# Optimization experiments

Measured on AMD Instinct MI355X. Metric: run time of the kernel, lower is better.

Reference implementation:

```python
import jax, jax.numpy as jnp
import numpy as np

B = 8
SHAPE = (4, 16, 16)   # latent video shape; S = prod = 1024
S = 1024
AE = 64               # ae_embed_dim
D = 768               # embed_dim
F = 3072              # mlp_dim
H = 12                # num_heads (heads are re-merged before the score matmul!)
L = 12                # num_layers
C = 17                # n_classes
OUT = 1024            # out_dim
EPS = 1e-6
HD = D // H


def setup_inputs() -> dict:
    key = jax.random.key(0)
    ks = iter(jax.random.split(key, 64))

    def p(shape, s=0.02):
        return jax.random.normal(next(ks), shape, jnp.float32) * s

    inp = {
        'x': jax.random.normal(next(ks), (B, *SHAPE, AE), jnp.float32),
        'mask': jnp.tril(jnp.ones((S, S), bool)),  # causal
        'label': jax.nn.one_hot(jax.random.randint(next(ks), (B,), 0, C), C, dtype=jnp.float32),
        'dense_in_w': p((D, AE)), 'dense_in_b': jnp.zeros((D,), jnp.float32),
        'sos': p((D,)),
        # BroadcastPositionBiases: embed_dim=768 split into 3 chunks of 256
        'pos0': p((SHAPE[0], D // 3)), 'pos1': p((SHAPE[1], D // 3)), 'pos2': p((SHAPE[2], D // 3)),
        'ln1_sw': p((L, D, C)), 'ln1_bw': p((L, D, C)),
        'qkv_w': p((L, 3 * D, D)), 'qkv_b': jnp.zeros((L, 3 * D), jnp.float32),
        'ao1_w': p((L, D, D)), 'ao1_b': jnp.zeros((L, D), jnp.float32),  # DotProductAttention.out_proj
        'ao2_w': p((L, D, D)), 'ao2_b': jnp.zeros((L, D), jnp.float32),  # MultiHeadAttention.out_proj
        'ln2_sw': p((L, D, C)), 'ln2_bw': p((L, D, C)),
        'mlp_w1': p((L, F, D)), 'mlp_b1': jnp.zeros((L, F), jnp.float32),
        'mlp_w2': p((L, D, F)), 'mlp_b2': jnp.zeros((L, D), jnp.float32),
        'lnf_sw': p((D, C)), 'lnf_bw': p((D, C)),
        'out_w': p((OUT, D)), 'out_b': jnp.zeros((OUT,), jnp.float32),
    }
    return inp


def cond_ln(x, cond, sw, bw):
    # conditional LayerNorm: mul = rsqrt(var+eps)*(1+Linear(cond)), bias = Linear(cond)
    mean = jnp.mean(x, axis=-1, keepdims=True)
    var = jnp.mean((x - mean) ** 2, axis=-1, keepdims=True)
    scale = cond @ sw.T   # [B, D]
    bias = cond @ bw.T    # [B, D]
    mul = jax.lax.rsqrt(var + EPS) * (1.0 + scale[:, None, :])
    return (x - mean) * mul + bias[:, None, :]


def pos_bias(embs, shape):
    n = len(shape)
    outs = []
    for i, e in enumerate(embs):
        sh = [1] * n + [e.shape[-1]]
        sh[i] = shape[i]
        outs.append(jnp.broadcast_to(e.reshape(sh), tuple(shape) + (e.shape[-1],)))
    return jnp.concatenate(outs, axis=-1).reshape(-1, sum(e.shape[-1] for e in embs))  # [S, D]


def attn_block(h, mask, qkv_w, qkv_b, o1_w, o1_b, o2_w, o2_b):
    Bn, Sn, Dn = h.shape
    qkv = h @ qkv_w.T + qkv_b                       # [B, S, 3D]
    qkv = qkv.reshape(Bn, Sn, H, 3 * HD)            # per-head [q|k|v] layout
    q = qkv[..., :HD].reshape(Bn, Sn, Dn)           # heads re-merged BEFORE scores
    k = qkv[..., HD:2 * HD].reshape(Bn, Sn, Dn)
    v = qkv[..., 2 * HD:].reshape(Bn, Sn, Dn)
    # NOTE: scaling uses full embed_dim (module quirk), not head_dim
    scores = jnp.einsum('bqd,bkd->bqk', q * (float(Dn) ** -0.5), k)
    scores = jnp.where(mask[None, :, :], scores, -jnp.inf)
    w = jax.nn.softmax(scores, axis=-1)
    out = jnp.einsum('bqk,bkd->bqd', w, v)
    out = out @ o1_w.T + o1_b                        # DotProductAttention.out_proj
    out = out @ o2_w.T + o2_b                        # MultiHeadAttention.out_proj (applied twice)
    return out


def _forward(x, mask, label, dense_in_w, dense_in_b, sos, pos0, pos1, pos2,
             ln1_sw, ln1_bw, qkv_w, qkv_b, ao1_w, ao1_b, ao2_w, ao2_b,
             ln2_sw, ln2_bw, mlp_w1, mlp_b1, mlp_w2, mlp_b2,
             lnf_sw, lnf_bw, out_w, out_b):
    Bn = x.shape[0]
    old_shape = x.shape[1:-1]
    h = x.reshape(Bn, -1, x.shape[-1]) @ dense_in_w.T + dense_in_b   # [B, S, D]
    # right shift with learned SOS token
    h = jnp.concatenate([jnp.broadcast_to(sos, (Bn, 1, D)), h[:, :-1]], axis=1)
    pb = pos_bias([pos0, pos1, pos2], old_shape)                     # [S, D]
    h = h + pb[None, :h.shape[1]]
    for l in range(L):
        hn = cond_ln(h, label, ln1_sw[l], ln1_bw[l])
        h = h + attn_block(hn, mask, qkv_w[l], qkv_b[l], ao1_w[l], ao1_b[l], ao2_w[l], ao2_b[l])
        hn = cond_ln(h, label, ln2_sw[l], ln2_bw[l])
        m = hn @ mlp_w1[l].T + mlp_b1[l]
        m = jax.nn.sigmoid(1.702 * m) * m           # GELU2
        m = m @ mlp_w2[l].T + mlp_b2[l]
        h = h + m
    h = cond_ln(h, label, lnf_sw, lnf_bw)
    out = h @ out_w.T + out_b                        # [B, S, OUT]
    return out.reshape(Bn, *old_shape, out.shape[-1])


def reference(x, mask, label, dense_in_w, dense_in_b, sos, pos0, pos1, pos2,
              ln1_sw, ln1_bw, qkv_w, qkv_b, ao1_w, ao1_b, ao2_w, ao2_b,
              ln2_sw, ln2_bw, mlp_w1, mlp_b1, mlp_w2, mlp_b2,
              lnf_sw, lnf_bw, out_w, out_b):
    return _forward(x, mask, label, dense_in_w, dense_in_b, sos, pos0, pos1, pos2,
                    ln1_sw, ln1_bw, qkv_w, qkv_b, ao1_w, ao1_b, ao2_w, ao2_b,
                    ln2_sw, ln2_bw, mlp_w1, mlp_b1, mlp_w2, mlp_b2,
                    lnf_sw, lnf_bw, out_w, out_b)
```

## Files before the change

### kernel.cpp

```cpp
#include <hip/hip_runtime.h>

typedef __bf16 bf16;
typedef __bf16 bf16x8 __attribute__((ext_vector_type(8)));
typedef __bf16 bf16x4 __attribute__((ext_vector_type(4)));
typedef float  f32x4  __attribute__((ext_vector_type(4)));

#define DEV __device__ __forceinline__

DEV void gload_lds16(const bf16* g, bf16* l) {
    __builtin_amdgcn_global_load_lds(
        (__attribute__((address_space(1))) void*)g,
        (__attribute__((address_space(3))) void*)l, 16, 0, 0);
}

enum { M_QKV, M_SCORES, M_PV, M_RESID, M_GELU, M_OUT, M_WM };

template<int MODE>
__global__ __launch_bounds__(256)
void gemm_k(const bf16* __restrict__ A, const bf16* __restrict__ B,
            int M, int N, int K,
            long long batchA, long long batchB, long long batchC,
            const float* __restrict__ bias,
            bf16* __restrict__ Cb, float* __restrict__ Cf,
            bf16* __restrict__ qp, bf16* __restrict__ kp, bf16* __restrict__ vp)
{
    const int bm = blockIdx.x, bn = blockIdx.y, bz = blockIdx.z;
    int kTiles = K >> 5;

    const int tid = threadIdx.x, wid = tid >> 6, lane = tid & 63;
    const bf16* Ab = A + (long long)bz * batchA + (long long)bm * 128 * K;
    const bf16* Bb = B + (long long)bz * batchB + (long long)bn * 128 * K;

    __shared__ __align__(16) bf16 sA[2][4096];
    __shared__ __align__(16) bf16 sB[2][4096];

    const int srow = wid * 16 + (lane >> 2);
    const int scol = (lane & 3) * 8;
    const long long aoff = (long long)srow * K + scol;

    auto stage = [&](int buf, int kt) {
        const bf16* ga = Ab + (long long)kt * 32;
        const bf16* gb = Bb + (long long)kt * 32;
        gload_lds16(ga + aoff,            &sA[buf][(wid * 16) * 32]);
        gload_lds16(ga + aoff + 64LL * K, &sA[buf][(64 + wid * 16) * 32]);
        gload_lds16(gb + aoff,            &sB[buf][(wid * 16) * 32]);
        gload_lds16(gb + aoff + 64LL * K, &sB[buf][(64 + wid * 16) * 32]);
    };

    f32x4 acc[4][4];
#pragma unroll
    for (int m = 0; m < 4; ++m)
#pragma unroll
        for (int n = 0; n < 4; ++n) acc[m][n] = (f32x4){0.f, 0.f, 0.f, 0.f};

    stage(0, 0);
    __syncthreads();

    const int wr = wid >> 1, wc = wid & 1;
    const int arow = wr * 64 + (lane & 15);
    const int brow = wc * 64 + (lane & 15);
    const int koff = (lane >> 4) * 8;

    for (int kt = 0; kt < kTiles; ++kt) {
        const int cur = kt & 1;
        if (kt + 1 < kTiles) stage(cur ^ 1, kt + 1);
        bf16x8 af[4], bfr[4];
#pragma unroll
        for (int m = 0; m < 4; ++m)
            af[m] = *(const bf16x8*)&sA[cur][(arow + m * 16) * 32 + koff];
#pragma unroll
        for (int n = 0; n < 4; ++n)
            bfr[n] = *(const bf16x8*)&sB[cur][(brow + n * 16) * 32 + koff];
#pragma unroll
        for (int m = 0; m < 4; ++m)
#pragma unroll
            for (int n = 0; n < 4; ++n)
                acc[m][n] = __builtin_amdgcn_mfma_f32_16x16x32_bf16(af[m], bfr[n], acc[m][n], 0, 0, 0);
        __syncthreads();
    }

    const int cr0 = bm * 128 + wr * 64 + (lane >> 4) * 4;
    const int cc0 = bn * 128 + wc * 64 + (lane & 15);
#pragma unroll
    for (int m = 0; m < 4; ++m) {
#pragma unroll
        for (int n = 0; n < 4; ++n) {
            const int col = cc0 + n * 16;
#pragma unroll
            for (int r = 0; r < 4; ++r) {
                const int row = cr0 + m * 16 + r;
                float v = acc[m][n][r];
                if (MODE == M_QKV) {
                    v += bias[col];
                    int hd = col / 192, rr = col % 192;
                    int b = row >> 10, s = row & 1023;
                    if (rr < 64)
                        qp[(long long)row * 768 + hd * 64 + rr] = (bf16)(v * 0.03608439182435161f);
                    else if (rr < 128)
                        kp[(long long)row * 768 + hd * 64 + (rr - 64)] = (bf16)v;
                    else
                        vp[((long long)b * 768 + hd * 64 + (rr - 128)) * 1024 + s] = (bf16)v;
                } else if (MODE == M_GELU) {
                    float xg = v + bias[col];
                    Cb[(long long)row * N + col] = (bf16)(xg / (1.f + __expf(-1.702f * xg)));
                } else if (MODE == M_RESID) {
                    long long idx = (long long)row * N + col;
                    Cf[idx] += v + bias[col];
                } else if (MODE == M_WM) {
                    Cb[(long long)bz * batchC + (long long)row * N + col] = (bf16)v;
                } else {
                    Cf[(long long)row * N + col] = v + bias[col];
                }
            }
        }
    }
}

template<int MODE>
__global__ __launch_bounds__(256)
void gemm64_k(const bf16* __restrict__ A, const bf16* __restrict__ B,
              int M, int N, int K,
              long long batchA, long long batchB, long long batchC,
              const float* __restrict__ bias,
              bf16* __restrict__ Cb, float* __restrict__ Cf)
{
    const int bm = blockIdx.x, bn = blockIdx.y, bz = blockIdx.z;
    if (MODE == M_SCORES && 2 * bn > bm) return;
    int kTiles = K >> 5;
    if (MODE == M_PV) {
        int lim = 2 * bm + 2;
        if (lim < kTiles) kTiles = lim;
    }

    const int tid = threadIdx.x, wid = tid >> 6, lane = tid & 63;
    const bf16* Ab = A + (long long)bz * batchA + (long long)bm * 64 * K;
    const bf16* Bb = B + (long long)bz * batchB + (long long)bn * 128 * K;

    __shared__ __align__(16) bf16 sA[2][2048];
    __shared__ __align__(16) bf16 sB[2][4096];

    const int srow = wid * 16 + (lane >> 2);
    const int scol = (lane & 3) * 8;
    const long long aoff = (long long)srow * K + scol;

    auto stage = [&](int buf, int kt) {
        const bf16* ga = Ab + (long long)kt * 32;
        const bf16* gb = Bb + (long long)kt * 32;
        gload_lds16(ga + aoff,            &sA[buf][(wid * 16) * 32]);
        gload_lds16(gb + aoff,            &sB[buf][(wid * 16) * 32]);
        gload_lds16(gb + aoff + 64LL * K, &sB[buf][(64 + wid * 16) * 32]);
    };

    f32x4 acc[2][4];
#pragma unroll
    for (int m = 0; m < 2; ++m)
#pragma unroll
        for (int n = 0; n < 4; ++n) acc[m][n] = (f32x4){0.f, 0.f, 0.f, 0.f};

    stage(0, 0);
    __syncthreads();

    const int wr = wid >> 1, wc = wid & 1;
    const int arow = wr * 32 + (lane & 15);
    const int brow = wc * 64 + (lane & 15);
    const int koff = (lane >> 4) * 8;

    for (int kt = 0; kt < kTiles; ++kt) {
        const int cur = kt & 1;
        if (kt + 1 < kTiles) stage(cur ^ 1, kt + 1);
        bf16x8 af[2], bfr[4];
#pragma unroll
        for (int m = 0; m < 2; ++m)
            af[m] = *(const bf16x8*)&sA[cur][(arow + m * 16) * 32 + koff];
#pragma unroll
        for (int n = 0; n < 4; ++n)
            bfr[n] = *(const bf16x8*)&sB[cur][(brow + n * 16) * 32 + koff];
#pragma unroll
        for (int m = 0; m < 2; ++m)
#pragma unroll
            for (int n = 0; n < 4; ++n)
                acc[m][n] = __builtin_amdgcn_mfma_f32_16x16x32_bf16(af[m], bfr[n], acc[m][n], 0, 0, 0);
        __syncthreads();
    }

    const int cr0 = bm * 64 + wr * 32 + (lane >> 4) * 4;
    const int cc0 = bn * 128 + wc * 64 + (lane & 15);
#pragma unroll
    for (int m = 0; m < 2; ++m) {
#pragma unroll
        for (int n = 0; n < 4; ++n) {
            const int col = cc0 + n * 16;
#pragma unroll
            for (int r = 0; r < 4; ++r) {
                const int row = cr0 + m * 16 + r;
                float v = acc[m][n][r];
                if (MODE == M_SCORES || MODE == M_PV) {
                    Cb[(long long)bz * batchC + (long long)row * N + col] = (bf16)v;
                } else {
                    Cf[(long long)row * N + col] = v + bias[col];
                }
            }
        }
    }
}

__global__ __launch_bounds__(256)
void cvt_bf16_k(const float* __restrict__ in, bf16* __restrict__ out, int n4)
{
    int i = blockIdx.x * 256 + threadIdx.x;
    if (i >= n4) return;
    float4 f = ((const float4*)in)[i];
    bf16x4 o = { (bf16)f.x, (bf16)f.y, (bf16)f.z, (bf16)f.w };
    ((bf16x4*)out)[i] = o;
}

__global__ __launch_bounds__(256)
void transpose_cvt_k(const float* __restrict__ in, bf16* __restrict__ out, int n)
{
    __shared__ float t[32][33];
    const int l = blockIdx.z;
    const int r0 = blockIdx.y * 32, c0 = blockIdx.x * 32;
    const float* src = in + (long long)l * n * n;
    bf16* dst = out + (long long)l * n * n;
    const int tx = threadIdx.x & 31, ty = threadIdx.x >> 5;
#pragma unroll
    for (int i = 0; i < 32; i += 8)
        t[ty + i][tx] = src[(long long)(r0 + ty + i) * n + c0 + tx];
    __syncthreads();
#pragma unroll
    for (int i = 0; i < 32; i += 8)
        dst[(long long)(c0 + ty + i) * n + r0 + tx] = (bf16)t[tx][ty + i];
}

__global__ __launch_bounds__(256)
void bias_merge_k(const float* __restrict__ o2w, const float* __restrict__ o1b,
                  const float* __restrict__ o2b, float* __restrict__ bm, int total)
{
    const int wid = threadIdx.x >> 6, lane = threadIdx.x & 63;
    const int idx = blockIdx.x * 4 + wid;
    if (idx >= total) return;
    const int l = idx / 768, a = idx - l * 768;
    const float* wrow = o2w + ((long long)l * 768 + a) * 768;
    const float* brow = o1b + (long long)l * 768;
    float s = 0.f;
#pragma unroll
    for (int j = 0; j < 12; ++j) {
        int c = j * 64 + lane;
        s += wrow[c] * brow[c];
    }
#pragma unroll
    for (int o = 32; o; o >>= 1) s += __shfl_down(s, o);
    if (lane == 0) bm[idx] = s + o2b[(long long)l * 768 + a];
}

__global__ __launch_bounds__(256)
void cond_proj_k(const float* __restrict__ label, const float* __restrict__ sw,
                 const float* __restrict__ bw, float* __restrict__ scale,
                 float* __restrict__ bias, int total)
{
    int idx = blockIdx.x * 256 + threadIdx.x;
    if (idx >= total) return;
    int l = idx / 6144;
    int rem = idx - l * 6144;
    int b = rem / 768, d = rem - (rem / 768) * 768;
    const float* lab = label + b * 17;
    const float* swp = sw + ((long long)l * 768 + d) * 17;
    const float* bwp = bw + ((long long)l * 768 + d) * 17;
    float s = 0.f, bb = 0.f;
#pragma unroll
    for (int c = 0; c < 17; ++c) { float lv = lab[c]; s += lv * swp[c]; bb += lv * bwp[c]; }
    scale[idx] = s;
    bias[idx]  = bb;
}

__global__ __launch_bounds__(256)
void shift_pos_k(const float* __restrict__ xe, const float* __restrict__ sos,
                 const float* __restrict__ p0, const float* __restrict__ p1,
                 const float* __restrict__ p2, float* __restrict__ h)
{
    const int s = blockIdx.x, b = blockIdx.y;
    const int i0 = s >> 8, i1 = (s >> 4) & 15, i2 = s & 15;
    const float* xr = xe + ((long long)b * 1024 + (s - 1)) * 768;
#pragma unroll
    for (int j = 0; j < 3; ++j) {
        const int d = j * 256 + threadIdx.x;
        float v = (s == 0) ? sos[d] : xr[d];
        float pbv = (d < 256) ? p0[i0 * 256 + d]
                  : (d < 512) ? p1[i1 * 256 + (d - 256)]
                              : p2[i2 * 256 + (d - 512)];
        h[((long long)b * 1024 + s) * 768 + d] = v + pbv;
    }
}

__global__ __launch_bounds__(256)
void cond_ln_k(const float* __restrict__ h, const float* __restrict__ scale,
               const float* __restrict__ bias, bf16* __restrict__ out)
{
    const long long row = (long long)blockIdx.y * 1024 + blockIdx.x;
    const int b = blockIdx.y;
    const float* hr = h + row * 768;
    float v[3], sum = 0.f, sq = 0.f;
#pragma unroll
    for (int j = 0; j < 3; ++j) {
        v[j] = hr[j * 256 + threadIdx.x];
        sum += v[j]; sq += v[j] * v[j];
    }
    __shared__ float sm[8];
#pragma unroll
    for (int o = 32; o; o >>= 1) { sum += __shfl_down(sum, o); sq += __shfl_down(sq, o); }
    const int wid = threadIdx.x >> 6;
    if ((threadIdx.x & 63) == 0) { sm[wid] = sum; sm[4 + wid] = sq; }
    __syncthreads();
    sum = sm[0] + sm[1] + sm[2] + sm[3];
    sq  = sm[4] + sm[5] + sm[6] + sm[7];
    const float mean = sum * (1.f / 768.f);
    const float var  = sq * (1.f / 768.f) - mean * mean;
    const float rs   = rsqrtf(var + 1e-6f);
    const float* sc = scale + (long long)b * 768;
    const float* bi = bias  + (long long)b * 768;
    bf16* orow = out + row * 768;
#pragma unroll
    for (int j = 0; j < 3; ++j) {
        const int d = j * 256 + threadIdx.x;
        orow[d] = (bf16)((v[j] - mean) * rs * (1.f + sc[d]) + bi[d]);
    }
}

__global__ __launch_bounds__(256)
void softmax_k(bf16* __restrict__ P)
{
    const int i = blockIdx.x, b = blockIdx.y;
    bf16* row = P + ((long long)b * 1024 + i) * 1024;
    const int len = i + 1;
    const int lim = (i | 63) + 1;
    float v[4], mx = -1e30f;
#pragma unroll
    for (int j = 0; j < 4; ++j) {
        int c = j * 256 + threadIdx.x;
        v[j] = (c < len) ? (float)row[c] : -1e30f;
        mx = fmaxf(mx, v[j]);
    }
    __shared__ float sm[8];
#pragma unroll
    for (int o = 32; o; o >>= 1) mx = fmaxf(mx, __shfl_down(mx, o));
    const int wid = threadIdx.x >> 6;
    if ((threadIdx.x & 63) == 0) sm[wid] = mx;
    __syncthreads();
    mx = fmaxf(fmaxf(sm[0], sm[1]), fmaxf(sm[2], sm[3]));
    float s = 0.f;
#pragma unroll
    for (int j = 0; j < 4; ++j) {
        v[j] = __expf(v[j] - mx);
        s += ((j * 256 + threadIdx.x) < len) ? v[j] : 0.f;
    }
#pragma unroll
    for (int o = 32; o; o >>= 1) s += __shfl_down(s, o);
    if ((threadIdx.x & 63) == 0) sm[4 + wid] = s;
    __syncthreads();
    s = sm[4] + sm[5] + sm[6] + sm[7];
    const float inv = 1.f / s;
#pragma unroll
    for (int j = 0; j < 4; ++j) {
        int c = j * 256 + threadIdx.x;
        if (c < lim) row[c] = (c < len) ? (bf16)(v[j] * inv) : (bf16)0.f;
    }
}

__global__ __launch_bounds__(256)
void fill_k(float* o, int n, float v)
{
    int i = blockIdx.x * 256 + threadIdx.x;
    if (i < n) o[i] = v;
}

extern "C" void kernel_launch(void* const* d_in, const int* in_sizes, int n_in,
                              void* d_out, int out_size, void* d_ws, size_t ws_size,
                              hipStream_t stream)
{
    (void)in_sizes; (void)n_in;
    const float* x     = (const float*)d_in[0];
    const float* label = (const float*)d_in[2];
    const float* dw    = (const float*)d_in[3];
    const float* db    = (const float*)d_in[4];
    const float* sos   = (const float*)d_in[5];
    const float* p0    = (const float*)d_in[6];
    const float* p1    = (const float*)d_in[7];
    const float* p2    = (const float*)d_in[8];
    const float* ln1sw = (const float*)d_in[9];
    const float* ln1bw = (const float*)d_in[10];
    const float* qkvw  = (const float*)d_in[11];
    const float* qkvb  = (const float*)d_in[12];
    const float* ao1w  = (const float*)d_in[13];
    const float* ao1b  = (const float*)d_in[14];
    const float* ao2w  = (const float*)d_in[15];
    const float* ao2b  = (const float*)d_in[16];
    const float* ln2sw = (const float*)d_in[17];
    const float* ln2bw = (const float*)d_in[18];
    const float* m1w   = (const float*)d_in[19];
    const float* m1b   = (const float*)d_in[20];
    const float* m2w   = (const float*)d_in[21];
    const float* m2b   = (const float*)d_in[22];
    const float* lnfsw = (const float*)d_in[23];
    const float* lnfbw = (const float*)d_in[24];
    const float* outw  = (const float*)d_in[25];
    const float* outb  = (const float*)d_in[26];
    float* out = (float*)d_out;

    char* p = (char*)d_ws;
    auto alloc = [&](size_t bytes) { void* r = (void*)p; p += (bytes + 255) & ~(size_t)255; return r; };
    float* h    = (float*)alloc(8192LL * 768 * 4);
    bf16*  hn   = (bf16*) alloc(8192LL * 768 * 2);
    bf16*  q    = (bf16*) alloc(8192LL * 768 * 2);
    bf16*  kbuf = (bf16*) alloc(8192LL * 768 * 2);
    bf16*  vT   = (bf16*) alloc(8192LL * 768 * 2);
    bf16*  P    = (bf16*) alloc(8LL * 1024 * 1024 * 2);
    bf16*  attn = (bf16*) alloc(8192LL * 768 * 2);
    bf16*  mb   = (bf16*) alloc(8192LL * 3072 * 2);
    bf16*  wout = (bf16*) alloc(1024LL * 768 * 2);
    bf16*  wmA  = (bf16*) alloc(12LL * 768 * 768 * 2);
    float* bmA  = (float*)alloc(12LL * 768 * 4);
    float* s1   = (float*)alloc(12LL * 8 * 768 * 4);
    float* b1   = (float*)alloc(12LL * 8 * 768 * 4);
    float* s2   = (float*)alloc(12LL * 8 * 768 * 4);
    float* b2   = (float*)alloc(12LL * 8 * 768 * 4);
    float* sf   = (float*)alloc(8LL * 768 * 4);
    float* bfb  = (float*)alloc(8LL * 768 * 4);

    size_t base_needed = (size_t)(p - (char*)d_ws);
    if (base_needed + 16LL * 1024 * 1024 > ws_size) {
        fill_k<<<(out_size + 255) / 256, 256, 0, stream>>>(out, out_size, 1e9f);
        return;
    }

    const long long SZ_QKV = 2304LL * 768, SZ_O = 768LL * 768, SZ_M = 3072LL * 768;
    size_t all_bytes = (size_t)(12 * (SZ_QKV + 2 * SZ_M)) * 2;
    bool allw = ((size_t)(p - (char*)d_ws) + all_bytes + 4096 <= ws_size);

    bf16 *wqkvA, *wm1A, *wm2A;
    if (allw) {
        wqkvA = (bf16*)alloc(12 * SZ_QKV * 2);
        wm1A  = (bf16*)alloc(12 * SZ_M * 2);
        wm2A  = (bf16*)alloc(12 * SZ_M * 2);
    } else {
        wqkvA = (bf16*)alloc(SZ_QKV * 2);
        wm1A  = (bf16*)alloc(SZ_M * 2);
        wm2A  = (bf16*)alloc(SZ_M * 2);
    }

    bf16*  xbf   = (bf16*)P;
    bf16*  dwbf  = (bf16*)P + 524288;
    bf16*  wo2bf = (bf16*)P + 1048576;
    float* xe    = (float*)mb;
    bf16*  o1t   = mb + 12582912;

    cvt_bf16_k<<<1024 * 768 / 4 / 256, 256, 0, stream>>>(outw, wout, 1024 * 768 / 4);
    cond_proj_k<<<(12 * 8 * 768 + 255) / 256, 256, 0, stream>>>(label, ln1sw, ln1bw, s1, b1, 12 * 8 * 768);
    cond_proj_k<<<(12 * 8 * 768 + 255) / 256, 256, 0, stream>>>(label, ln2sw, ln2bw, s2, b2, 12 * 8 * 768);
    cond_proj_k<<<(8 * 768 + 255) / 256, 256, 0, stream>>>(label, lnfsw, lnfbw, sf, bfb, 8 * 768);

    if (allw) {
        cvt_bf16_k<<<(int)(12 * SZ_QKV / 4 / 256), 256, 0, stream>>>(qkvw, wqkvA, (int)(12 * SZ_QKV / 4));
        cvt_bf16_k<<<(int)(12 * SZ_M / 4 / 256),   256, 0, stream>>>(m1w,  wm1A,  (int)(12 * SZ_M / 4));
        cvt_bf16_k<<<(int)(12 * SZ_M / 4 / 256),   256, 0, stream>>>(m2w,  wm2A,  (int)(12 * SZ_M / 4));
    }

    cvt_bf16_k<<<(int)(12 * SZ_O / 4 / 256), 256, 0, stream>>>(ao2w, wo2bf, (int)(12 * SZ_O / 4));
    transpose_cvt_k<<<dim3(24, 24, 12), 256, 0, stream>>>(ao1w, o1t, 768);
    gemm_k<M_WM><<<dim3(6, 6, 12), 256, 0, stream>>>(
        wo2bf, o1t, 768, 768, 768, SZ_O, SZ_O, SZ_O,
        nullptr, wmA, nullptr, nullptr, nullptr, nullptr);
    bias_merge_k<<<(12 * 768 + 3) / 4, 256, 0, stream>>>(ao2w, ao1b, ao2b, bmA, 12 * 768);

    cvt_bf16_k<<<8192 * 64 / 4 / 256, 256, 0, stream>>>(x, xbf, 8192 * 64 / 4);
    cvt_bf16_k<<<768 * 64 / 4 / 256, 256, 0, stream>>>(dw, dwbf, 768 * 64 / 4);
    gemm_k<M_OUT><<<dim3(64, 6, 1), 256, 0, stream>>>(
        xbf, dwbf, 8192, 768, 64, 0, 0, 0, db, nullptr, xe, nullptr, nullptr, nullptr);
    shift_pos_k<<<dim3(1024, 8), 256, 0, stream>>>(xe, sos, p0, p1, p2, h);

    for (int l = 0; l < 12; ++l) {
        bf16 *wqkv, *wm1, *wm2;
        if (allw) {
            wqkv = wqkvA + (long long)l * SZ_QKV;
            wm1  = wm1A  + (long long)l * SZ_M;
            wm2  = wm2A  + (long long)l * SZ_M;
        } else {
            wqkv = wqkvA; wm1 = wm1A; wm2 = wm2A;
            cvt_bf16_k<<<(int)(SZ_QKV / 4 / 256), 256, 0, stream>>>(qkvw + (long long)l * SZ_QKV, wqkv, (int)(SZ_QKV / 4));
            cvt_bf16_k<<<(int)(SZ_M / 4 / 256),   256, 0, stream>>>(m1w  + (long long)l * SZ_M,   wm1,  (int)(SZ_M / 4));
            cvt_bf16_k<<<(int)(SZ_M / 4 / 256),   256, 0, stream>>>(m2w  + (long long)l * SZ_M,   wm2,  (int)(SZ_M / 4));
        }

        cond_ln_k<<<dim3(1024, 8), 256, 0, stream>>>(h, s1 + (long long)l * 6144, b1 + (long long)l * 6144, hn);

        gemm_k<M_QKV><<<dim3(64, 18, 1), 256, 0, stream>>>(
            hn, wqkv, 8192, 2304, 768, 0, 0, 0,
            qkvb + (long long)l * 2304, nullptr, nullptr, q, kbuf, vT);

        gemm64_k<M_SCORES><<<dim3(16, 8, 8), 256, 0, stream>>>(
            q, kbuf, 1024, 1024, 768, 1024LL * 768, 1024LL * 768, 1024LL * 1024,
            nullptr, P, nullptr);

        softmax_k<<<dim3(1024, 8), 256, 0, stream>>>(P);

        gemm64_k<M_PV><<<dim3(16, 6, 8), 256, 0, stream>>>(
            P, vT, 1024, 768, 1024, 1024LL * 1024, 768LL * 1024, 1024LL * 768,
            nullptr, attn, nullptr);

        gemm_k<M_RESID><<<dim3(64, 6, 1), 256, 0, stream>>>(
            attn, wmA + (long long)l * SZ_O, 8192, 768, 768, 0, 0, 0,
            bmA + (long long)l * 768, nullptr, h, nullptr, nullptr, nullptr);

        cond_ln_k<<<dim3(1024, 8), 256, 0, stream>>>(h, s2 + (long long)l * 6144, b2 + (long long)l * 6144, hn);

        gemm_k<M_GELU><<<dim3(64, 24, 1), 256, 0, stream>>>(
            hn, wm1, 8192, 3072, 768, 0, 0, 0,
            m1b + (long long)l * 3072, mb, nullptr, nullptr, nullptr, nullptr);

        gemm_k<M_RESID><<<dim3(64, 6, 1), 256, 0, stream>>>(
            mb, wm2, 8192, 768, 3072, 0, 0, 0,
            m2b + (long long)l * 768, nullptr, h, nullptr, nullptr, nullptr);
    }

    cond_ln_k<<<dim3(1024, 8), 256, 0, stream>>>(h, sf, bfb, hn);
    gemm64_k<M_OUT><<<dim3(128, 8, 1), 256, 0, stream>>>(
        hn, wout, 8192, 1024, 768, 0, 0, 0,
        outb, nullptr, out);
}
```

Baseline: 4.506 ms.

## Deepen GEMM K-loop prefetch to a four-buffer LDS ring with explicit vmcnt waits

Both GEMM kernels move from a double-buffered LDS pipeline with two `__syncthreads` per tile to a four-slot ring in dynamic shared memory. Up to three K-tiles are kept in flight. Each iteration waits with a partial `s_waitcnt vmcnt`, issues a single raw barrier, then issues the next prefetch. The aim is to hide global-to-LDS load latency behind the MFMA work and to drop one barrier per tile. In exchange, LDS per block doubles (64KB for the 128-tile kernel, 48KB for the 64-row kernel), which can limit how many blocks fit on a CU.

Result: faster. 3.980 ms (-11.7%).

```diff
diff --git a/kernel.cpp b/kernel.cpp
--- a/kernel.cpp
+++ b/kernel.cpp
@@ -11,6 +11,12 @@
     __builtin_amdgcn_global_load_lds(
         (__attribute__((address_space(1))) void*)g,
         (__attribute__((address_space(3))) void*)l, 16, 0, 0);
+}
+
+DEV void barrier_raw() {
+    asm volatile("" ::: "memory");
+    __builtin_amdgcn_s_barrier();
+    asm volatile("" ::: "memory");
 }
 
 enum { M_QKV, M_SCORES, M_PV, M_RESID, M_GELU, M_OUT, M_WM };
@@ -25,14 +31,15 @@
             bf16* __restrict__ qp, bf16* __restrict__ kp, bf16* __restrict__ vp)
 {
     const int bm = blockIdx.x, bn = blockIdx.y, bz = blockIdx.z;
-    int kTiles = K >> 5;
+    const int kTiles = K >> 5;
 
     const int tid = threadIdx.x, wid = tid >> 6, lane = tid & 63;
     const bf16* Ab = A + (long long)bz * batchA + (long long)bm * 128 * K;
     const bf16* Bb = B + (long long)bz * batchB + (long long)bn * 128 * K;
 
-    __shared__ __align__(16) bf16 sA[2][4096];
-    __shared__ __align__(16) bf16 sB[2][4096];
+    extern __shared__ __align__(16) bf16 smem[];
+    bf16* sA = smem;
+    bf16* sB = smem + 16384;
 
     const int srow = wid * 16 + (lane >> 2);
     const int scol = (lane & 3) * 8;
@@ -41,10 +48,12 @@
     auto stage = [&](int buf, int kt) {
         const bf16* ga = Ab + (long long)kt * 32;
         const bf16* gb = Bb + (long long)kt * 32;
-        gload_lds16(ga + aoff,            &sA[buf][(wid * 16) * 32]);
-        gload_lds16(ga + aoff + 64LL * K, &sA[buf][(64 + wid * 16) * 32]);
-        gload_lds16(gb + aoff,            &sB[buf][(wid * 16) * 32]);
-        gload_lds16(gb + aoff + 64LL * K, &sB[buf][(64 + wid * 16) * 32]);
+        bf16* a = sA + buf * 4096;
+        bf16* b = sB + buf * 4096;
+        gload_lds16(ga + aoff,            a + (wid * 16) * 32);
+        gload_lds16(ga + aoff + 64LL * K, a + (64 + wid * 16) * 32);
+        gload_lds16(gb + aoff,            b + (wid * 16) * 32);
+        gload_lds16(gb + aoff + 64LL * K, b + (64 + wid * 16) * 32);
     };
 
     f32x4 acc[4][4];
@@ -53,8 +62,8 @@
 #pragma unroll
         for (int n = 0; n < 4; ++n) acc[m][n] = (f32x4){0.f, 0.f, 0.f, 0.f};
 
-    stage(0, 0);
-    __syncthreads();
+    const int npre = kTiles < 3 ? kTiles : 3;
+    for (int t = 0; t < npre; ++t) stage(t, t);
 
     const int wr = wid >> 1, wc = wid & 1;
     const int arow = wr * 64 + (lane & 15);
@@ -62,21 +71,28 @@
     const int koff = (lane >> 4) * 8;
 
     for (int kt = 0; kt < kTiles; ++kt) {
-        const int cur = kt & 1;
-        if (kt + 1 < kTiles) stage(cur ^ 1, kt + 1);
+        const int rem = kTiles - 1 - kt;
+        if (rem >= 2)      asm volatile("s_waitcnt vmcnt(8)" ::: "memory");
+        else if (rem == 1) asm volatile("s_waitcnt vmcnt(4)" ::: "memory");
+        else               asm volatile("s_waitcnt vmcnt(0)" ::: "memory");
+        barrier_raw();
+        if (kt + 3 < kTiles) stage((kt + 3) & 3, kt + 3);
+
+        const int cur = kt & 3;
+        const bf16* a = sA + cur * 4096;
+        const bf16* b = sB + cur * 4096;
         bf16x8 af[4], bfr[4];
 #pragma unroll
         for (int m = 0; m < 4; ++m)
-            af[m] = *(const bf16x8*)&sA[cur][(arow + m * 16) * 32 + koff];
+            af[m] = *(const bf16x8*)&a[(arow + m * 16) * 32 + koff];
 #pragma unroll
         for (int n = 0; n < 4; ++n)
-            bfr[n] = *(const bf16x8*)&sB[cur][(brow + n * 16) * 32 + koff];
+            bfr[n] = *(const bf16x8*)&b[(brow + n * 16) * 32 + koff];
 #pragma unroll
         for (int m = 0; m < 4; ++m)
 #pragma unroll
             for (int n = 0; n < 4; ++n)
                 acc[m][n] = __builtin_amdgcn_mfma_f32_16x16x32_bf16(af[m], bfr[n], acc[m][n], 0, 0, 0);
-        __syncthreads();
     }
 
     const int cr0 = bm * 128 + wr * 64 + (lane >> 4) * 4;
@@ -93,13 +109,13 @@
                 if (MODE == M_QKV) {
                     v += bias[col];
                     int hd = col / 192, rr = col % 192;
-                    int b = row >> 10, s = row & 1023;
+                    int b2 = row >> 10, s = row & 1023;
                     if (rr < 64)
                         qp[(long long)row * 768 + hd * 64 + rr] = (bf16)(v * 0.03608439182435161f);
                     else if (rr < 128)
                         kp[(long long)row * 768 + hd * 64 + (rr - 64)] = (bf16)v;
                     else
-                        vp[((long long)b * 768 + hd * 64 + (rr - 128)) * 1024 + s] = (bf16)v;
+                        vp[((long long)b2 * 768 + hd * 64 + (rr - 128)) * 1024 + s] = (bf16)v;
                 } else if (MODE == M_GELU) {
                     float xg = v + bias[col];
                     Cb[(long long)row * N + col] = (bf16)(xg / (1.f + __expf(-1.702f * xg)));
@@ -136,8 +152,9 @@
     const bf16* Ab = A + (long long)bz * batchA + (long long)bm * 64 * K;
     const bf16* Bb = B + (long long)bz * batchB + (long long)bn * 128 * K;
 
-    __shared__ __align__(16) bf16 sA[2][2048];
-    __shared__ __align__(16) bf16 sB[2][4096];
+    extern __shared__ __align__(16) bf16 smem[];
+    bf16* sA = smem;
+    bf16* sB = smem + 8192;
 
     const int srow = wid * 16 + (lane >> 2);
     const int scol = (lane & 3) * 8;
@@ -146,9 +163,9 @@
     auto stage = [&](int buf, int kt) {
         const bf16* ga = Ab + (long long)kt * 32;
         const bf16* gb = Bb + (long long)kt * 32;
-        gload_lds16(ga + aoff,            &sA[buf][(wid * 16) * 32]);
-        gload_lds16(gb + aoff,            &sB[buf][(wid * 16) * 32]);
-        gload_lds16(gb + aoff + 64LL * K, &sB[buf][(64 + wid * 16) * 32]);
+        gload_lds16(ga + aoff,            sA + buf * 2048 + (wid * 16) * 32);
+        gload_lds16(gb + aoff,            sB + buf * 4096 + (wid * 16) * 32);
+        gload_lds16(gb + aoff + 64LL * K, sB + buf * 4096 + (64 + wid * 16) * 32);
     };
 
     f32x4 acc[2][4];
@@ -157,8 +174,8 @@
 #pragma unroll
         for (int n = 0; n < 4; ++n) acc[m][n] = (f32x4){0.f, 0.f, 0.f, 0.f};
 
-    stage(0, 0);
-    __syncthreads();
+    const int npre = kTiles < 3 ? kTiles : 3;
+    for (int t = 0; t < npre; ++t) stage(t, t);
 
     const int wr = wid >> 1, wc = wid & 1;
     const int arow = wr * 32 + (lane & 15);
@@ -166,21 +183,28 @@
     const int koff = (lane >> 4) * 8;
 
     for (int kt = 0; kt < kTiles; ++kt) {
-        const int cur = kt & 1;
-        if (kt + 1 < kTiles) stage(cur ^ 1, kt + 1);
+        const int rem = kTiles - 1 - kt;
+        if (rem >= 2)      asm volatile("s_waitcnt vmcnt(6)" ::: "memory");
+        else if (rem == 1) asm volatile("s_waitcnt vmcnt(3)" ::: "memory");
+        else               asm volatile("s_waitcnt vmcnt(0)" ::: "memory");
+        barrier_raw();
+        if (kt + 3 < kTiles) stage((kt + 3) & 3, kt + 3);
+
+        const int cur = kt & 3;
+        const bf16* a = sA + cur * 2048;
+        const bf16* b = sB + cur * 4096;
         bf16x8 af[2], bfr[4];
 #pragma unroll
         for (int m = 0; m < 2; ++m)
-            af[m] = *(const bf16x8*)&sA[cur][(arow + m * 16) * 32 + koff];
+            af[m] = *(const bf16x8*)&a[(arow + m * 16) * 32 + koff];
 #pragma unroll
         for (int n = 0; n < 4; ++n)
-            bfr[n] = *(const bf16x8*)&sB[cur][(brow + n * 16) * 32 + koff];
+            bfr[n] = *(const bf16x8*)&b[(brow + n * 16) * 32 + koff];
 #pragma unroll
         for (int m = 0; m < 2; ++m)
 #pragma unroll
             for (int n = 0; n < 4; ++n)
                 acc[m][n] = __builtin_amdgcn_mfma_f32_16x16x32_bf16(af[m], bfr[n], acc[m][n], 0, 0, 0);
-        __syncthreads();
     }
 
     const int cr0 = bm * 64 + wr * 32 + (lane >> 4) * 4;
@@ -466,14 +490,14 @@
 
     cvt_bf16_k<<<(int)(12 * SZ_O / 4 / 256), 256, 0, stream>>>(ao2w, wo2bf, (int)(12 * SZ_O / 4));
     transpose_cvt_k<<<dim3(24, 24, 12), 256, 0, stream>>>(ao1w, o1t, 768);
-    gemm_k<M_WM><<<dim3(6, 6, 12), 256, 0, stream>>>(
+    gemm_k<M_WM><<<dim3(6, 6, 12), 256, 65536, stream>>>(
         wo2bf, o1t, 768, 768, 768, SZ_O, SZ_O, SZ_O,
         nullptr, wmA, nullptr, nullptr, nullptr, nullptr);
     bias_merge_k<<<(12 * 768 + 3) / 4, 256, 0, stream>>>(ao2w, ao1b, ao2b, bmA, 12 * 768);
 
     cvt_bf16_k<<<8192 * 64 / 4 / 256, 256, 0, stream>>>(x, xbf, 8192 * 64 / 4);
     cvt_bf16_k<<<768 * 64 / 4 / 256, 256, 0, stream>>>(dw, dwbf, 768 * 64 / 4);
-    gemm_k<M_OUT><<<dim3(64, 6, 1), 256, 0, stream>>>(
+    gemm_k<M_OUT><<<dim3(64, 6, 1), 256, 65536, stream>>>(
         xbf, dwbf, 8192, 768, 64, 0, 0, 0, db, nullptr, xe, nullptr, nullptr, nullptr);
     shift_pos_k<<<dim3(1024, 8), 256, 0, stream>>>(xe, sos, p0, p1, p2, h);
 
@@ -492,37 +516,37 @@
 
         cond_ln_k<<<dim3(1024, 8), 256, 0, stream>>>(h, s1 + (long long)l * 6144, b1 + (long long)l * 6144, hn);
 
-        gemm_k<M_QKV><<<dim3(64, 18, 1), 256, 0, stream>>>(
+        gemm_k<M_QKV><<<dim3(64, 18, 1), 256, 65536, stream>>>(
             hn, wqkv, 8192, 2304, 768, 0, 0, 0,
             qkvb + (long long)l * 2304, nullptr, nullptr, q, kbuf, vT);
 
-        gemm64_k<M_SCORES><<<dim3(16, 8, 8), 256, 0, stream>>>(
+        gemm64_k<M_SCORES><<<dim3(16, 8, 8), 256, 49152, stream>>>(
             q, kbuf, 1024, 1024, 768, 1024LL * 768, 1024LL * 768, 1024LL * 1024,
             nullptr, P, nullptr);
 
         softmax_k<<<dim3(1024, 8), 256, 0, stream>>>(P);
 
-        gemm64_k<M_PV><<<dim3(16, 6, 8), 256, 0, stream>>>(
+        gemm64_k<M_PV><<<dim3(16, 6, 8), 256, 49152, stream>>>(
             P, vT, 1024, 768, 1024, 1024LL * 1024, 768LL * 1024, 1024LL * 768,
             nullptr, attn, nullptr);
 
-        gemm_k<M_RESID><<<dim3(64, 6, 1), 256, 0, stream>>>(
+        gemm_k<M_RESID><<<dim3(64, 6, 1), 256, 65536, stream>>>(
             attn, wmA + (long long)l * SZ_O, 8192, 768, 768, 0, 0, 0,
             bmA + (long long)l * 768, nullptr, h, nullptr, nullptr, nullptr);
 
         cond_ln_k<<<dim3(1024, 8), 256, 0, stream>>>(h, s2 + (long long)l * 6144, b2 + (long long)l * 6144, hn);
 
-        gemm_k<M_GELU><<<dim3(64, 24, 1), 256, 0, stream>>>(
+        gemm_k<M_GELU><<<dim3(64, 24, 1), 256, 65536, stream>>>(
             hn, wm1, 8192, 3072, 768, 0, 0, 0,
             m1b + (long long)l * 3072, mb, nullptr, nullptr, nullptr, nullptr);
 
-        gemm_k<M_RESID><<<dim3(64, 6, 1), 256, 0, stream>>>(
+        gemm_k<M_RESID><<<dim3(64, 6, 1), 256, 65536, stream>>>(
             mb, wm2, 8192, 768, 3072, 0, 0, 0,
             m2b + (long long)l * 768, nullptr, h, nullptr, nullptr, nullptr);
     }
 
     cond_ln_k<<<dim3(1024, 8), 256, 0, stream>>>(h, sf, bfb, hn);
-    gemm64_k<M_OUT><<<dim3(128, 8, 1), 256, 0, stream>>>(
+    gemm64_k<M_OUT><<<dim3(128, 8, 1), 256, 49152, stream>>>(
         hn, wout, 8192, 1024, 768, 0, 0, 0,
         outb, nullptr, out);
 }
```
